# Kernel optimization log

Measured on AMD Instinct MI355X. Metric: run time of the kernel, lower is better.

The kernel has to match this reference:

```python
import jax, jax.numpy as jnp
import numpy as np


def lstm_step(x_t, h, c, Wih, Whh, bih, bhh):
    # PyTorch LSTM gate order: i, f, g, o
    gates = x_t @ Wih.T + h @ Whh.T + bih + bhh
    i, f, g, o = jnp.split(gates, 4, axis=-1)
    i = jax.nn.sigmoid(i)
    f = jax.nn.sigmoid(f)
    g = jnp.tanh(g)
    o = jax.nn.sigmoid(o)
    c_new = f * c + i * g
    h_new = o * jnp.tanh(c_new)
    return h_new, c_new


def setup_inputs() -> dict:
    key = jax.random.key(0)
    N, C, T, V, M = 512, 3, 300, 25, 2
    F = C * V * M  # 150
    H = 100
    ks = jax.random.split(key, 12)
    s = 1.0 / np.sqrt(H)  # PyTorch LSTM/Linear init scale
    u = lambda k, shape: jax.random.uniform(k, shape, jnp.float32, -s, s)
    return {
        "x": jax.random.normal(ks[0], (N, C, T, V, M), jnp.float32),
        "enc_Wih": u(ks[1], (4 * H, F)),
        "enc_Whh": u(ks[2], (4 * H, H)),
        "enc_bih": u(ks[3], (4 * H,)),
        "enc_bhh": u(ks[4], (4 * H,)),
        "dec_Wih": u(ks[5], (4 * H, F)),
        "dec_Whh": u(ks[6], (4 * H, H)),
        "dec_bih": u(ks[7], (4 * H,)),
        "dec_bhh": u(ks[8], (4 * H,)),
        "fc_W": u(ks[9], (F, H)),
        "fc_b": u(ks[10], (F,)),
    }


def reference(x, enc_Wih, enc_Whh, enc_bih, enc_bhh,
              dec_Wih, dec_Whh, dec_bih, dec_bhh, fc_W, fc_b):
    N, C, T, V, M = x.shape
    F = C * V * M
    H = enc_Whh.shape[1]
    # (N,C,T,V,M) -> (N,T,C*V*M)
    xs = jnp.transpose(x, (0, 2, 1, 3, 4)).reshape(N, T, F)

    # Encoder LSTM: only need final (h, c)
    h0 = jnp.zeros((N, H), x.dtype)
    c0 = jnp.zeros((N, H), x.dtype)

    def enc_step(carry, xt):
        h, c = carry
        h, c = lstm_step(xt, h, c, enc_Wih, enc_Whh, enc_bih, enc_bhh)
        return (h, c), None

    (h, c), _ = jax.lax.scan(enc_step, (h0, c0), jnp.swapaxes(xs, 0, 1))

    inp0 = jnp.zeros((N, F), x.dtype)

    def dec_step(carry, _):
        inp, h, c = carry
        h, c = lstm_step(inp, h, c, dec_Wih, dec_Whh, dec_bih, dec_bhh)
        out = h @ fc_W.T + fc_b
        return (out, h, c), out

    _, outs = jax.lax.scan(dec_step, (inp0, h, c), None, length=T - 1)  # [T-1,N,F]

    # outputs[:,0,:] stays zero, like the torch.zeros buffer
    outputs = jnp.concatenate([jnp.zeros((1, N, F), x.dtype), outs], axis=0)  # [T,N,F]
    outputs = jnp.swapaxes(outputs, 0, 1).reshape(N, T, C, V, M)
    return jnp.transpose(outputs, (0, 2, 1, 3, 4))  # (N,C,T,V,M)
```

## Files before the change

### kernel.cpp

```cpp
#include <hip/hip_runtime.h>
#include <hip/hip_fp16.h>


#define B_W2P   0u
#define B_WDP   102400u
#define B_WEP   204800u
#define B_PIH   307200u
#define B_BENC  460800u
#define B_B1    462848u
#define B_BEFF  464896u
#define B_HIST  466944u
#define HIST_STRIDE 29952
#define B_XG    31137792u

typedef _Float16 h2_t __attribute__((ext_vector_type(2)));

#if defined(__has_builtin)
#if __has_builtin(__builtin_amdgcn_fdot2)
#define HAS_FDOT2 1
#endif
#endif

__device__ __forceinline__ float fdot2u(unsigned a, unsigned b, float c) {
#ifdef HAS_FDOT2
  return __builtin_amdgcn_fdot2(__builtin_bit_cast(h2_t, a), __builtin_bit_cast(h2_t, b), c, false);
#else
  float al = __half2float(__ushort_as_half((unsigned short)(a & 0xffffu)));
  float ah = __half2float(__ushort_as_half((unsigned short)(a >> 16)));
  float bl = __half2float(__ushort_as_half((unsigned short)(b & 0xffffu)));
  float bh = __half2float(__ushort_as_half((unsigned short)(b >> 16)));
  return fmaf(ah, bh, fmaf(al, bl, c));
#endif
}

__device__ __forceinline__ unsigned pack2f(float a, float b) {
  return (unsigned)__half_as_ushort(__float2half(a)) |
         ((unsigned)__half_as_ushort(__float2half(b)) << 16);
}

__device__ __forceinline__ float fast_sig(float x) {
  float e = __builtin_amdgcn_exp2f(x * -1.442695040888963f);
  return __builtin_amdgcn_rcpf(1.f + e);
}
__device__ __forceinline__ float fast_tanh(float x) {
  float e = __builtin_amdgcn_exp2f(x * -2.885390081777926f);
  return fmaf(2.f, __builtin_amdgcn_rcpf(1.f + e), -1.f);
}

__device__ __forceinline__ float lstm_tail(float acc, int ty, float& c) {
  float sg = fast_sig(acc);
  float th = fast_tanh(acc);
  float act = (ty == 2) ? th : sg;
  float v1 = __shfl_xor(act, 1);
  float v2 = __shfl_xor(act, 2);
  float v3 = __shfl_xor(v1, 2);
  c = fmaf(v1, c, act * v2);
  return v3 * fast_tanh(c);
}

__device__ __forceinline__ float dot100(const unsigned short* hb, const unsigned* wp) {
  const uint4* h4 = (const uint4*)hb;
  float a0 = 0.f, a1 = 0.f, a2 = 0.f, a3 = 0.f;
#pragma unroll
  for (int ch = 0; ch < 12; ++ch) {
    uint4 v = h4[ch];
    a0 = fdot2u(wp[4 * ch + 0], v.x, a0);
    a1 = fdot2u(wp[4 * ch + 1], v.y, a1);
    a2 = fdot2u(wp[4 * ch + 2], v.z, a2);
    a3 = fdot2u(wp[4 * ch + 3], v.w, a3);
  }
  uint2 v2 = *(const uint2*)(hb + 96);
  a0 = fdot2u(wp[48], v2.x, a0);
  a1 = fdot2u(wp[49], v2.y, a1);
  return (a0 + a1) + (a2 + a3);
}

__global__ void prep(const float* __restrict__ dWih, const float* __restrict__ dWhh,
                     const float* __restrict__ dbih, const float* __restrict__ dbhh,
                     const float* __restrict__ eWih, const float* __restrict__ eWhh,
                     const float* __restrict__ ebih, const float* __restrict__ ebhh,
                     const float* __restrict__ fcW,  const float* __restrict__ fcb,
                     char* __restrict__ wsb)
{
  int idx = blockIdx.x * 256 + threadIdx.x;
  if (idx < 25600) {
    int q = idx >> 9, t = idx & 511;
    unsigned w2p = 0, wdp = 0, wep = 0;
    if (t < 400) {
      int r = (t & 3) * 100 + (t >> 2);
      int j0 = 2 * q, j1 = 2 * q + 1;
      float wd0 = dWhh[r * 100 + j0], wd1 = dWhh[r * 100 + j1];
      float we0 = eWhh[r * 100 + j0], we1 = eWhh[r * 100 + j1];
      float s0 = 0.f, s1 = 0.f;
      for (int f = 0; f < 150; ++f) {
        float a = dWih[r * 150 + f];
        s0 = fmaf(a, fcW[f * 100 + j0], s0);
        s1 = fmaf(a, fcW[f * 100 + j1], s1);
      }
      w2p = pack2f(wd0 + s0, wd1 + s1);
      wdp = pack2f(wd0, wd1);
      wep = pack2f(we0, we1);
    }
    ((unsigned*)(wsb + B_W2P))[idx] = w2p;
    ((unsigned*)(wsb + B_WDP))[idx] = wdp;
    ((unsigned*)(wsb + B_WEP))[idx] = wep;
  } else if (idx < 25600 + 38400) {
    int k = idx - 25600; int d = k >> 9, t = k & 511;
    unsigned pk = 0;
    if (t < 400) {
      int r = (t & 3) * 100 + (t >> 2);
      pk = pack2f(eWih[r * 150 + 2 * d], eWih[r * 150 + 2 * d + 1]);
    }
    ((unsigned*)(wsb + B_PIH))[k] = pk;
  } else if (idx < 25600 + 38400 + 512) {
    int t = idx - (25600 + 38400);
    float be = 0.f, b1 = 0.f, bf = 0.f;
    if (t < 400) {
      int r = (t & 3) * 100 + (t >> 2);
      be = ebih[r] + ebhh[r];
      b1 = dbih[r] + dbhh[r];
      float acc = 0.f;
      for (int f = 0; f < 150; ++f) acc = fmaf(dWih[r * 150 + f], fcb[f], acc);
      bf = b1 + acc;
    }
    ((float*)(wsb + B_BENC))[t] = be;
    ((float*)(wsb + B_B1))[t]   = b1;
    ((float*)(wsb + B_BEFF))[t] = bf;
  }
}

__global__ __launch_bounds__(512, 4)
void pre(const float* __restrict__ x, const char* __restrict__ wsb,
         unsigned short* __restrict__ xg, int n0)
{
  const int tid = threadIdx.x;
  const int n = n0 + blockIdx.x;
  __shared__ unsigned short xls[150 * 160];

  unsigned wih[75];
  const unsigned* pih = (const unsigned*)(wsb + B_PIH);
#pragma unroll
  for (int d = 0; d < 75; ++d) wih[d] = pih[(d << 9) + tid];

  const float* xb = x + (size_t)n * 45000;
  unsigned short* xgr = xg + (size_t)blockIdx.x * 120000 + ((tid < 400) ? tid : 0);
  const bool on = tid < 400;

  for (int phase = 0; phase < 2; ++phase) {
    const int tbase = phase * 150;
    if (phase) __syncthreads();
    for (int d = tid; d < 150 * 160; d += 512) {
      int tl = d / 160, f = d - tl * 160;
      float v = 0.f;
      if (f < 150) {
        int c = f / 50, q = f - c * 50;
        v = xb[c * 15000 + (tbase + tl) * 50 + q];
      }
      xls[tl * 160 + f] = __half_as_ushort(__float2half(v));
    }
    __syncthreads();
    if (on) {
      for (int tl = 0; tl < 150; ++tl) {
        const uint4* row = (const uint4*)(xls + tl * 160);
        float a0 = 0.f, a1 = 0.f, a2 = 0.f, a3 = 0.f;
#pragma unroll
        for (int ch = 0; ch < 18; ++ch) {
          uint4 v = row[ch];
          a0 = fdot2u(wih[4 * ch + 0], v.x, a0);
          a1 = fdot2u(wih[4 * ch + 1], v.y, a1);
          a2 = fdot2u(wih[4 * ch + 2], v.z, a2);
          a3 = fdot2u(wih[4 * ch + 3], v.w, a3);
        }
        uint4 v = row[18];
        a0 = fdot2u(wih[72], v.x, a0);
        a1 = fdot2u(wih[73], v.y, a1);
        a2 = fdot2u(wih[74], v.z, a2);
        float a = (a0 + a1) + (a2 + a3);
        xgr[(size_t)(tbase + tl) * 400] = __half_as_ushort(__float2half(a));
      }
    }
  }
}

__global__ __launch_bounds__(512, 4)
void recurrent(const unsigned short* __restrict__ xg, char* __restrict__ wsb, int n0)
{
  const int t  = threadIdx.x;
  const int n  = n0 + blockIdx.x;
  const int j  = t >> 2, ty = t & 3;
  const bool leader = (t < 400) && (ty == 0);
  __shared__ unsigned short hh[2][112];

  const unsigned* WEP = (const unsigned*)(wsb + B_WEP);
  const unsigned* WDP = (const unsigned*)(wsb + B_WDP);
  const unsigned* W2P = (const unsigned*)(wsb + B_W2P);

  unsigned wp[50];
#pragma unroll
  for (int q = 0; q < 50; ++q) wp[q] = WEP[(q << 9) + t];

  const float benc = ((const float*)(wsb + B_BENC))[t];
  const float b1g  = ((const float*)(wsb + B_B1))[t];
  const float beff = ((const float*)(wsb + B_BEFF))[t];
  unsigned short* histn = (unsigned short*)(wsb + B_HIST) + (size_t)n * HIST_STRIDE;
  const unsigned short* xgr = xg + (size_t)blockIdx.x * 120000 + ((t < 400) ? t : 0);
  float c = 0.f;

  unsigned short p1 = xgr[400];
  {
    float acc = benc + __half2float(__ushort_as_half(xgr[0]));
    float hn = lstm_tail(acc, ty, c);
    if (leader) hh[1][j] = __half_as_ushort(__float2half(hn));
    __syncthreads();
  }
  for (int ts = 1; ts < 300; ++ts) {
    const int rd = ts & 1, wr = rd ^ 1;
    unsigned short pn = xgr[(size_t)((ts + 1 < 300) ? ts + 1 : 299) * 400];
    float acc = benc + __half2float(__ushort_as_half(p1)) + dot100(hh[rd], wp);
    float hn = lstm_tail(acc, ty, c);
    if (leader) hh[wr][j] = __half_as_ushort(__float2half(hn));
    __syncthreads();
    p1 = pn;
  }

#pragma unroll
  for (int q = 0; q < 50; ++q) wp[q] = WDP[(q << 9) + t];
  {
    float acc = b1g + dot100(hh[0], wp);
    float hn = lstm_tail(acc, ty, c);
    if (leader) {
      hh[1][j] = __half_as_ushort(__float2half(hn));
      histn[j] = __half_as_ushort(__float2half(hn));
    }
    __syncthreads();
  }
#pragma unroll
  for (int q = 0; q < 50; ++q) wp[q] = W2P[(q << 9) + t];
  for (int s = 2; s <= 299; ++s) {
    const int rd = (299 + s) & 1, wr = rd ^ 1;
    float acc = beff + dot100(hh[rd], wp);
    float hn = lstm_tail(acc, ty, c);
    if (leader) {
      hh[wr][j] = __half_as_ushort(__float2half(hn));
      histn[(s - 1) * 100 + j] = __half_as_ushort(__float2half(hn));
    }
    __syncthreads();
  }
}

__global__ __launch_bounds__(192, 4)
void emit(const char* __restrict__ wsb, const float* __restrict__ fcW,
          const float* __restrict__ fcb, float* __restrict__ out)
{
  const int f = threadIdx.x;
  const int n = blockIdx.x;
  const int z = blockIdx.y;
  __shared__ unsigned short hl[15008];

  const uint4* src = (const uint4*)((const unsigned short*)(wsb + B_HIST) +
                                    (size_t)n * HIST_STRIDE + z * 15000);
  for (int k = f; k < 1875; k += 192) ((uint4*)hl)[k] = src[k];

  const bool on = f < 150;
  unsigned fw[50];
  float bias = 0.f;
  if (on) {
    const float* fp = fcW + f * 100;
#pragma unroll
    for (int q = 0; q < 50; ++q) fw[q] = pack2f(fp[2 * q], fp[2 * q + 1]);
    bias = fcb[f];
  }
  __syncthreads();

  if (!on) return;
  const int cc = f / 50, r = f - cc * 50;
  float* ob = out + (size_t)n * 45000 + cc * 15000 + r;
  if (z == 0) ob[0] = 0.f;
  const int rows = z ? 149 : 150;
  for (int tl = 0; tl < rows; ++tl) {
    const uint4* row = (const uint4*)(hl + tl * 100);
    float a0 = bias, a1 = 0.f, a2 = 0.f, a3 = 0.f;
#pragma unroll
    for (int ch = 0; ch < 12; ++ch) {
      uint4 v = row[ch];
      a0 = fdot2u(fw[4 * ch + 0], v.x, a0);
      a1 = fdot2u(fw[4 * ch + 1], v.y, a1);
      a2 = fdot2u(fw[4 * ch + 2], v.z, a2);
      a3 = fdot2u(fw[4 * ch + 3], v.w, a3);
    }
    uint2 v2 = *(const uint2*)(hl + tl * 100 + 96);
    a0 = fdot2u(fw[48], v2.x, a0);
    a1 = fdot2u(fw[49], v2.y, a1);
    const int tt = z * 150 + tl + 1;
    ob[tt * 50] = (a0 + a1) + (a2 + a3);
  }
}

extern "C" void kernel_launch(void* const* d_in, const int* in_sizes, int n_in,
                              void* d_out, int out_size, void* d_ws, size_t ws_size,
                              hipStream_t stream) {
  const float* x    = (const float*)d_in[0];
  const float* eWih = (const float*)d_in[1];
  const float* eWhh = (const float*)d_in[2];
  const float* ebih = (const float*)d_in[3];
  const float* ebhh = (const float*)d_in[4];
  const float* dWih = (const float*)d_in[5];
  const float* dWhh = (const float*)d_in[6];
  const float* dbih = (const float*)d_in[7];
  const float* dbhh = (const float*)d_in[8];
  const float* fcW  = (const float*)d_in[9];
  const float* fcb  = (const float*)d_in[10];
  float* out = (float*)d_out;
  char* wsb  = (char*)d_ws;

  int npass = 1;
  while (npass < 8) {
    size_t need = (size_t)B_XG + (size_t)(512 / npass) * 300 * 400 * 2;
    if (need <= ws_size) break;
    npass *= 2;
  }
  const int chunk = 512 / npass;
  unsigned short* xg = (unsigned short*)(wsb + B_XG);

  prep<<<252, 256, 0, stream>>>(dWih, dWhh, dbih, dbhh, eWih, eWhh, ebih, ebhh, fcW, fcb, wsb);
  for (int p = 0; p < npass; ++p) {
    pre<<<chunk, 512, 0, stream>>>(x, wsb, xg, p * chunk);
    recurrent<<<chunk, 512, 0, stream>>>(xg, wsb, p * chunk);
  }
  emit<<<dim3(512, 2), 192, 0, stream>>>(wsb, fcW, fcb, out);
}
```

Baseline: 1.141 ms.

## Split encoder along time into two halves over all sequences instead of batch passes

Instead of running the pre/recurrent pair once per batch chunk, sized to the workspace, the encoder input projection and recurrence are split into two time halves of 150 steps. Each half launches all 512 sequences at once, and the h and c state is saved to and restored from the history area between the halves. This keeps the xg buffer at half the full size while giving every launch the whole batch, which cuts the serial recurrent step chain when multiple passes were needed before. It costs an extra launch pair plus a state save and reload when the workspace could previously hold the whole buffer in one pass. It also no longer checks ws_size.

Result: slower. 1.219 ms (+6.8%).

```diff
diff --git a/kernel.cpp b/kernel.cpp
--- a/kernel.cpp
+++ b/kernel.cpp
@@ -131,10 +131,10 @@
 
 __global__ __launch_bounds__(512, 4)
 void pre(const float* __restrict__ x, const char* __restrict__ wsb,
-         unsigned short* __restrict__ xg, int n0)
+         unsigned short* __restrict__ xg, int tbase)
 {
   const int tid = threadIdx.x;
-  const int n = n0 + blockIdx.x;
+  const int n = blockIdx.x;
   __shared__ unsigned short xls[150 * 160];
 
   unsigned wih[75];
@@ -143,50 +143,46 @@
   for (int d = 0; d < 75; ++d) wih[d] = pih[(d << 9) + tid];
 
   const float* xb = x + (size_t)n * 45000;
-  unsigned short* xgr = xg + (size_t)blockIdx.x * 120000 + ((tid < 400) ? tid : 0);
+  unsigned short* xgr = xg + (size_t)n * 60000 + ((tid < 400) ? tid : 0);
   const bool on = tid < 400;
 
-  for (int phase = 0; phase < 2; ++phase) {
-    const int tbase = phase * 150;
-    if (phase) __syncthreads();
-    for (int d = tid; d < 150 * 160; d += 512) {
-      int tl = d / 160, f = d - tl * 160;
-      float v = 0.f;
-      if (f < 150) {
-        int c = f / 50, q = f - c * 50;
-        v = xb[c * 15000 + (tbase + tl) * 50 + q];
+  for (int d = tid; d < 150 * 160; d += 512) {
+    int tl = d / 160, f = d - tl * 160;
+    float v = 0.f;
+    if (f < 150) {
+      int c = f / 50, q = f - c * 50;
+      v = xb[c * 15000 + (tbase + tl) * 50 + q];
+    }
+    xls[tl * 160 + f] = __half_as_ushort(__float2half(v));
+  }
+  __syncthreads();
+  if (on) {
+    for (int tl = 0; tl < 150; ++tl) {
+      const uint4* row = (const uint4*)(xls + tl * 160);
+      float a0 = 0.f, a1 = 0.f, a2 = 0.f, a3 = 0.f;
+#pragma unroll
+      for (int ch = 0; ch < 18; ++ch) {
+        uint4 v = row[ch];
+        a0 = fdot2u(wih[4 * ch + 0], v.x, a0);
+        a1 = fdot2u(wih[4 * ch + 1], v.y, a1);
+        a2 = fdot2u(wih[4 * ch + 2], v.z, a2);
+        a3 = fdot2u(wih[4 * ch + 3], v.w, a3);
       }
-      xls[tl * 160 + f] = __half_as_ushort(__float2half(v));
-    }
-    __syncthreads();
-    if (on) {
-      for (int tl = 0; tl < 150; ++tl) {
-        const uint4* row = (const uint4*)(xls + tl * 160);
-        float a0 = 0.f, a1 = 0.f, a2 = 0.f, a3 = 0.f;
-#pragma unroll
-        for (int ch = 0; ch < 18; ++ch) {
-          uint4 v = row[ch];
-          a0 = fdot2u(wih[4 * ch + 0], v.x, a0);
-          a1 = fdot2u(wih[4 * ch + 1], v.y, a1);
-          a2 = fdot2u(wih[4 * ch + 2], v.z, a2);
-          a3 = fdot2u(wih[4 * ch + 3], v.w, a3);
-        }
-        uint4 v = row[18];
-        a0 = fdot2u(wih[72], v.x, a0);
-        a1 = fdot2u(wih[73], v.y, a1);
-        a2 = fdot2u(wih[74], v.z, a2);
-        float a = (a0 + a1) + (a2 + a3);
-        xgr[(size_t)(tbase + tl) * 400] = __half_as_ushort(__float2half(a));
-      }
+      uint4 v = row[18];
+      a0 = fdot2u(wih[72], v.x, a0);
+      a1 = fdot2u(wih[73], v.y, a1);
+      a2 = fdot2u(wih[74], v.z, a2);
+      float a = (a0 + a1) + (a2 + a3);
+      xgr[(size_t)tl * 400] = __half_as_ushort(__float2half(a));
     }
   }
 }
 
 __global__ __launch_bounds__(512, 4)
-void recurrent(const unsigned short* __restrict__ xg, char* __restrict__ wsb, int n0)
+void recurrent(const unsigned short* __restrict__ xg, char* __restrict__ wsb, int phase)
 {
   const int t  = threadIdx.x;
-  const int n  = n0 + blockIdx.x;
+  const int n  = blockIdx.x;
   const int j  = t >> 2, ty = t & 3;
   const bool leader = (t < 400) && (ty == 0);
   __shared__ unsigned short hh[2][112];
@@ -203,19 +199,41 @@
   const float b1g  = ((const float*)(wsb + B_B1))[t];
   const float beff = ((const float*)(wsb + B_BEFF))[t];
   unsigned short* histn = (unsigned short*)(wsb + B_HIST) + (size_t)n * HIST_STRIDE;
-  const unsigned short* xgr = xg + (size_t)blockIdx.x * 120000 + ((t < 400) ? t : 0);
+  float* stc = (float*)(histn + 128);
+  const unsigned short* xgr = xg + (size_t)n * 60000 + ((t < 400) ? t : 0);
   float c = 0.f;
 
-  unsigned short p1 = xgr[400];
-  {
-    float acc = benc + __half2float(__ushort_as_half(xgr[0]));
-    float hn = lstm_tail(acc, ty, c);
-    if (leader) hh[1][j] = __half_as_ushort(__float2half(hn));
-    __syncthreads();
-  }
-  for (int ts = 1; ts < 300; ++ts) {
+  if (phase == 0) {
+    unsigned short p1 = xgr[400];
+    {
+      float acc = benc + __half2float(__ushort_as_half(xgr[0]));
+      float hn = lstm_tail(acc, ty, c);
+      if (leader) hh[1][j] = __half_as_ushort(__float2half(hn));
+      __syncthreads();
+    }
+    for (int ts = 1; ts < 150; ++ts) {
+      const int rd = ts & 1, wr = rd ^ 1;
+      unsigned short pn = xgr[(size_t)((ts + 1 < 150) ? ts + 1 : 149) * 400];
+      float acc = benc + __half2float(__ushort_as_half(p1)) + dot100(hh[rd], wp);
+      float hn = lstm_tail(acc, ty, c);
+      if (leader) hh[wr][j] = __half_as_ushort(__float2half(hn));
+      __syncthreads();
+      p1 = pn;
+    }
+    if (t < 100) histn[t] = hh[0][t];
+    if (leader)  stc[j] = c;
+    return;
+  }
+
+  if (t < 100) hh[0][t] = histn[t];
+  if (t < 400) c = stc[j];
+  unsigned short p1 = xgr[0];
+  __syncthreads();
+
+  for (int ts = 150; ts < 300; ++ts) {
     const int rd = ts & 1, wr = rd ^ 1;
-    unsigned short pn = xgr[(size_t)((ts + 1 < 300) ? ts + 1 : 299) * 400];
+    const int idx = ts - 150;
+    unsigned short pn = xgr[(size_t)((idx + 1 < 150) ? idx + 1 : 149) * 400];
     float acc = benc + __half2float(__ushort_as_half(p1)) + dot100(hh[rd], wp);
     float hn = lstm_tail(acc, ty, c);
     if (leader) hh[wr][j] = __half_as_ushort(__float2half(hn));
@@ -313,19 +331,12 @@
   float* out = (float*)d_out;
   char* wsb  = (char*)d_ws;
 
-  int npass = 1;
-  while (npass < 8) {
-    size_t need = (size_t)B_XG + (size_t)(512 / npass) * 300 * 400 * 2;
-    if (need <= ws_size) break;
-    npass *= 2;
-  }
-  const int chunk = 512 / npass;
   unsigned short* xg = (unsigned short*)(wsb + B_XG);
 
   prep<<<252, 256, 0, stream>>>(dWih, dWhh, dbih, dbhh, eWih, eWhh, ebih, ebhh, fcW, fcb, wsb);
-  for (int p = 0; p < npass; ++p) {
-    pre<<<chunk, 512, 0, stream>>>(x, wsb, xg, p * chunk);
-    recurrent<<<chunk, 512, 0, stream>>>(xg, wsb, p * chunk);
-  }
+  pre<<<512, 512, 0, stream>>>(x, wsb, xg, 0);
+  recurrent<<<512, 512, 0, stream>>>(xg, wsb, 0);
+  pre<<<512, 512, 0, stream>>>(x, wsb, xg, 150);
+  recurrent<<<512, 512, 0, stream>>>(xg, wsb, 1);
   emit<<<dim3(512, 2), 192, 0, stream>>>(wsb, fcW, fcb, out);
 }
```

## Batch 16 samples per block with MFMA and fuse input projection into recurrence

Applied to the files above, without the earlier changes.

The separate input-projection kernel and its fp16 gate buffer in workspace are removed. The recurrent kernel now processes 16 batch samples per block. It concatenates h and x_t along K and computes all gates with 16x16x32 f16 MFMA instructions, while raw x for the next step is prefetched and converted into shared memory. This removes the large intermediate write and read and the extra launch, and moves the gate matvec onto the matrix cores. The cost is a grid of only 32 blocks, which uses few CUs, plus wider per-step work on each wave.

Result: slower. 1.200 ms (+5.1%).

```diff
diff --git a/kernel.cpp b/kernel.cpp
--- a/kernel.cpp
+++ b/kernel.cpp
@@ -11,9 +11,10 @@
 #define B_BEFF  464896u
 #define B_HIST  466944u
 #define HIST_STRIDE 29952
-#define B_XG    31137792u
 
 typedef _Float16 h2_t __attribute__((ext_vector_type(2)));
+typedef _Float16 f16x8 __attribute__((ext_vector_type(8)));
+typedef float f32x4v __attribute__((ext_vector_type(4)));
 
 #if defined(__has_builtin)
 #if __has_builtin(__builtin_amdgcn_fdot2)
@@ -47,32 +48,9 @@
   return fmaf(2.f, __builtin_amdgcn_rcpf(1.f + e), -1.f);
 }
 
-__device__ __forceinline__ float lstm_tail(float acc, int ty, float& c) {
-  float sg = fast_sig(acc);
-  float th = fast_tanh(acc);
-  float act = (ty == 2) ? th : sg;
-  float v1 = __shfl_xor(act, 1);
-  float v2 = __shfl_xor(act, 2);
-  float v3 = __shfl_xor(v1, 2);
-  c = fmaf(v1, c, act * v2);
-  return v3 * fast_tanh(c);
-}
-
-__device__ __forceinline__ float dot100(const unsigned short* hb, const unsigned* wp) {
-  const uint4* h4 = (const uint4*)hb;
-  float a0 = 0.f, a1 = 0.f, a2 = 0.f, a3 = 0.f;
-#pragma unroll
-  for (int ch = 0; ch < 12; ++ch) {
-    uint4 v = h4[ch];
-    a0 = fdot2u(wp[4 * ch + 0], v.x, a0);
-    a1 = fdot2u(wp[4 * ch + 1], v.y, a1);
-    a2 = fdot2u(wp[4 * ch + 2], v.z, a2);
-    a3 = fdot2u(wp[4 * ch + 3], v.w, a3);
-  }
-  uint2 v2 = *(const uint2*)(hb + 96);
-  a0 = fdot2u(wp[48], v2.x, a0);
-  a1 = fdot2u(wp[49], v2.y, a1);
-  return (a0 + a1) + (a2 + a3);
+__device__ __forceinline__ f32x4v mfma16(uint4 a, uint4 b, f32x4v c) {
+  return __builtin_amdgcn_mfma_f32_16x16x32_f16(
+      __builtin_bit_cast(f16x8, a), __builtin_bit_cast(f16x8, b), c, 0, 0, 0);
 }
 
 __global__ void prep(const float* __restrict__ dWih, const float* __restrict__ dWhh,
@@ -129,120 +107,192 @@
   }
 }
 
-__global__ __launch_bounds__(512, 4)
-void pre(const float* __restrict__ x, const char* __restrict__ wsb,
-         unsigned short* __restrict__ xg, int n0)
+__global__ __launch_bounds__(448, 2)
+void recurrent(const float* __restrict__ x, char* __restrict__ wsb)
 {
-  const int tid = threadIdx.x;
-  const int n = n0 + blockIdx.x;
-  __shared__ unsigned short xls[150 * 160];
-
-  unsigned wih[75];
-  const unsigned* pih = (const unsigned*)(wsb + B_PIH);
-#pragma unroll
-  for (int d = 0; d < 75; ++d) wih[d] = pih[(d << 9) + tid];
-
-  const float* xb = x + (size_t)n * 45000;
-  unsigned short* xgr = xg + (size_t)blockIdx.x * 120000 + ((tid < 400) ? tid : 0);
-  const bool on = tid < 400;
-
-  for (int phase = 0; phase < 2; ++phase) {
-    const int tbase = phase * 150;
-    if (phase) __syncthreads();
-    for (int d = tid; d < 150 * 160; d += 512) {
-      int tl = d / 160, f = d - tl * 160;
-      float v = 0.f;
-      if (f < 150) {
-        int c = f / 50, q = f - c * 50;
-        v = xb[c * 15000 + (tbase + tl) * 50 + q];
-      }
-      xls[tl * 160 + f] = __half_as_ushort(__float2half(v));
-    }
-    __syncthreads();
-    if (on) {
-      for (int tl = 0; tl < 150; ++tl) {
-        const uint4* row = (const uint4*)(xls + tl * 160);
-        float a0 = 0.f, a1 = 0.f, a2 = 0.f, a3 = 0.f;
-#pragma unroll
-        for (int ch = 0; ch < 18; ++ch) {
-          uint4 v = row[ch];
-          a0 = fdot2u(wih[4 * ch + 0], v.x, a0);
-          a1 = fdot2u(wih[4 * ch + 1], v.y, a1);
-          a2 = fdot2u(wih[4 * ch + 2], v.z, a2);
-          a3 = fdot2u(wih[4 * ch + 3], v.w, a3);
-        }
-        uint4 v = row[18];
-        a0 = fdot2u(wih[72], v.x, a0);
-        a1 = fdot2u(wih[73], v.y, a1);
-        a2 = fdot2u(wih[74], v.z, a2);
-        float a = (a0 + a1) + (a2 + a3);
-        xgr[(size_t)(tbase + tl) * 400] = __half_as_ushort(__float2half(a));
-      }
-    }
-  }
-}
-
-__global__ __launch_bounds__(512, 4)
-void recurrent(const unsigned short* __restrict__ xg, char* __restrict__ wsb, int n0)
-{
-  const int t  = threadIdx.x;
-  const int n  = n0 + blockIdx.x;
-  const int j  = t >> 2, ty = t & 3;
-  const bool leader = (t < 400) && (ty == 0);
-  __shared__ unsigned short hh[2][112];
+  const int tid  = threadIdx.x;
+  const int w    = tid >> 6;
+  const int lane = tid & 63;
+  const int sp   = lane & 15;
+  const int q    = lane >> 4;
+  const int nb   = blockIdx.x * 16;
+
+  __shared__ unsigned short hx[2][16][264];
+  for (int k = tid; k < 2 * 16 * 264; k += 448) ((unsigned short*)hx)[k] = 0;
 
   const unsigned* WEP = (const unsigned*)(wsb + B_WEP);
   const unsigned* WDP = (const unsigned*)(wsb + B_WDP);
   const unsigned* W2P = (const unsigned*)(wsb + B_W2P);
-
-  unsigned wp[50];
-#pragma unroll
-  for (int q = 0; q < 50; ++q) wp[q] = WEP[(q << 9) + t];
-
-  const float benc = ((const float*)(wsb + B_BENC))[t];
-  const float b1g  = ((const float*)(wsb + B_B1))[t];
-  const float beff = ((const float*)(wsb + B_BEFF))[t];
-  unsigned short* histn = (unsigned short*)(wsb + B_HIST) + (size_t)n * HIST_STRIDE;
-  const unsigned short* xgr = xg + (size_t)blockIdx.x * 120000 + ((t < 400) ? t : 0);
-  float c = 0.f;
-
-  unsigned short p1 = xgr[400];
+  const unsigned* PIH = (const unsigned*)(wsb + B_PIH);
+
+  const int nt = (w < 4) ? 4 : 3;
+  int cells[4];
+  float4 bs[4];
+  uint4 af[4][8];
+#pragma unroll
+  for (int i = 0; i < 4; ++i) {
+    const int tile = (i < nt) ? (w + 7 * i) : 0;
+    const int col = tile * 16 + sp;
+    cells[i] = 4 * tile + q;
+#pragma unroll
+    for (int kk = 0; kk < 8; ++kk) {
+      unsigned e[4];
+#pragma unroll
+      for (int l = 0; l < 4; ++l) {
+        const int p = kk * 16 + q * 4 + l;
+        unsigned v = 0u;
+        if (p < 50) v = WEP[p * 512 + col];
+        else if (p < 125) v = PIH[(p - 50) * 512 + col];
+        e[l] = v;
+      }
+      af[i][kk] = make_uint4(e[0], e[1], e[2], e[3]);
+    }
+    bs[i] = ((const float4*)(wsb + B_BENC))[cells[i]];
+  }
+
+  const bool stg = tid < 400;
+  const int ssp = tid / 25;
+  const int sr  = tid - ssp * 25;
+  const float* xb = x + (size_t)(nb + (stg ? ssp : 0)) * 45000;
+  int soff[6];
+#pragma unroll
+  for (int l = 0; l < 6; ++l) {
+    const int f = sr * 6 + l;
+    const int cd = f / 50;
+    soff[l] = cd * 15000 + (f - cd * 50);
+  }
+  const int sdst = (stg ? ssp : 0) * 264 + 100 + sr * 6;
+
+  unsigned short* histn = (unsigned short*)(wsb + B_HIST) + (size_t)(nb + sp) * HIST_STRIDE;
+
+  __syncthreads();
+  if (stg) {
+    float xv[6];
+#pragma unroll
+    for (int l = 0; l < 6; ++l) xv[l] = xb[soff[l]];
+    unsigned short* d = &hx[0][0][0] + sdst;
+    *(unsigned*)(d + 0) = pack2f(xv[0], xv[1]);
+    *(unsigned*)(d + 2) = pack2f(xv[2], xv[3]);
+    *(unsigned*)(d + 4) = pack2f(xv[4], xv[5]);
+  }
+  __syncthreads();
+
+  float cst[4] = {0.f, 0.f, 0.f, 0.f};
+
+  for (int t = 0; t < 300; ++t) {
+    const int rd = t & 1, wr = rd ^ 1;
+    const bool pf = stg && (t < 299);
+    float xv[6];
+    if (pf) {
+      const int to = (t + 1) * 50;
+#pragma unroll
+      for (int l = 0; l < 6; ++l) xv[l] = xb[soff[l] + to];
+    }
+    f32x4v acc[4];
+#pragma unroll
+    for (int i = 0; i < 4; ++i) {
+      acc[i][0] = bs[i].x; acc[i][1] = bs[i].y;
+      acc[i][2] = bs[i].z; acc[i][3] = bs[i].w;
+    }
+#pragma unroll
+    for (int kk = 0; kk < 8; ++kk) {
+      uint4 b = *(const uint4*)(&hx[rd][sp][kk * 32 + q * 8]);
+#pragma unroll
+      for (int i = 0; i < 4; ++i)
+        if (i < nt) acc[i] = mfma16(af[i][kk], b, acc[i]);
+    }
+#pragma unroll
+    for (int i = 0; i < 4; ++i) {
+      if (i < nt) {
+        float ii = fast_sig(acc[i][0]), ff = fast_sig(acc[i][1]);
+        float gg = fast_tanh(acc[i][2]), oo = fast_sig(acc[i][3]);
+        cst[i] = fmaf(ff, cst[i], ii * gg);
+        float h = oo * fast_tanh(cst[i]);
+        hx[wr][sp][cells[i]] = __half_as_ushort(__float2half(h));
+      }
+    }
+    if (pf) {
+      unsigned short* d = &hx[wr][0][0] + sdst;
+      *(unsigned*)(d + 0) = pack2f(xv[0], xv[1]);
+      *(unsigned*)(d + 2) = pack2f(xv[2], xv[3]);
+      *(unsigned*)(d + 4) = pack2f(xv[4], xv[5]);
+    }
+    __syncthreads();
+  }
+
+  auto loadA4 = [&](const unsigned* W, unsigned bofs) {
+#pragma unroll
+    for (int i = 0; i < 4; ++i) {
+      const int tile = (i < nt) ? (w + 7 * i) : 0;
+      const int col = tile * 16 + sp;
+#pragma unroll
+      for (int kk = 0; kk < 4; ++kk) {
+        unsigned e[4];
+#pragma unroll
+        for (int l = 0; l < 4; ++l) {
+          const int p = kk * 16 + q * 4 + l;
+          e[l] = (p < 50) ? W[p * 512 + col] : 0u;
+        }
+        af[i][kk] = make_uint4(e[0], e[1], e[2], e[3]);
+      }
+      bs[i] = ((const float4*)(wsb + bofs))[cells[i]];
+    }
+  };
+
+  loadA4(WDP, B_B1);
   {
-    float acc = benc + __half2float(__ushort_as_half(xgr[0]));
-    float hn = lstm_tail(acc, ty, c);
-    if (leader) hh[1][j] = __half_as_ushort(__float2half(hn));
+    f32x4v acc[4];
+#pragma unroll
+    for (int i = 0; i < 4; ++i) {
+      acc[i][0] = bs[i].x; acc[i][1] = bs[i].y;
+      acc[i][2] = bs[i].z; acc[i][3] = bs[i].w;
+    }
+#pragma unroll
+    for (int kk = 0; kk < 4; ++kk) {
+      uint4 b = *(const uint4*)(&hx[0][sp][kk * 32 + q * 8]);
+#pragma unroll
+      for (int i = 0; i < 4; ++i)
+        if (i < nt) acc[i] = mfma16(af[i][kk], b, acc[i]);
+    }
+#pragma unroll
+    for (int i = 0; i < 4; ++i) {
+      if (i < nt) {
+        float ii = fast_sig(acc[i][0]), ff = fast_sig(acc[i][1]);
+        float gg = fast_tanh(acc[i][2]), oo = fast_sig(acc[i][3]);
+        cst[i] = fmaf(ff, cst[i], ii * gg);
+        float h = oo * fast_tanh(cst[i]);
+        hx[1][sp][cells[i]] = __half_as_ushort(__float2half(h));
+        histn[cells[i]] = __half_as_ushort(__float2half(h));
+      }
+    }
     __syncthreads();
   }
-  for (int ts = 1; ts < 300; ++ts) {
-    const int rd = ts & 1, wr = rd ^ 1;
-    unsigned short pn = xgr[(size_t)((ts + 1 < 300) ? ts + 1 : 299) * 400];
-    float acc = benc + __half2float(__ushort_as_half(p1)) + dot100(hh[rd], wp);
-    float hn = lstm_tail(acc, ty, c);
-    if (leader) hh[wr][j] = __half_as_ushort(__float2half(hn));
-    __syncthreads();
-    p1 = pn;
-  }
-
-#pragma unroll
-  for (int q = 0; q < 50; ++q) wp[q] = WDP[(q << 9) + t];
-  {
-    float acc = b1g + dot100(hh[0], wp);
-    float hn = lstm_tail(acc, ty, c);
-    if (leader) {
-      hh[1][j] = __half_as_ushort(__float2half(hn));
-      histn[j] = __half_as_ushort(__float2half(hn));
-    }
-    __syncthreads();
-  }
-#pragma unroll
-  for (int q = 0; q < 50; ++q) wp[q] = W2P[(q << 9) + t];
+  loadA4(W2P, B_BEFF);
   for (int s = 2; s <= 299; ++s) {
     const int rd = (299 + s) & 1, wr = rd ^ 1;
-    float acc = beff + dot100(hh[rd], wp);
-    float hn = lstm_tail(acc, ty, c);
-    if (leader) {
-      hh[wr][j] = __half_as_ushort(__float2half(hn));
-      histn[(s - 1) * 100 + j] = __half_as_ushort(__float2half(hn));
+    f32x4v acc[4];
+#pragma unroll
+    for (int i = 0; i < 4; ++i) {
+      acc[i][0] = bs[i].x; acc[i][1] = bs[i].y;
+      acc[i][2] = bs[i].z; acc[i][3] = bs[i].w;
+    }
+#pragma unroll
+    for (int kk = 0; kk < 4; ++kk) {
+      uint4 b = *(const uint4*)(&hx[rd][sp][kk * 32 + q * 8]);
+#pragma unroll
+      for (int i = 0; i < 4; ++i)
+        if (i < nt) acc[i] = mfma16(af[i][kk], b, acc[i]);
+    }
+#pragma unroll
+    for (int i = 0; i < 4; ++i) {
+      if (i < nt) {
+        float ii = fast_sig(acc[i][0]), ff = fast_sig(acc[i][1]);
+        float gg = fast_tanh(acc[i][2]), oo = fast_sig(acc[i][3]);
+        cst[i] = fmaf(ff, cst[i], ii * gg);
+        float h = oo * fast_tanh(cst[i]);
+        hx[wr][sp][cells[i]] = __half_as_ushort(__float2half(h));
+        histn[(s - 1) * 100 + cells[i]] = __half_as_ushort(__float2half(h));
+      }
     }
     __syncthreads();
   }
@@ -313,19 +363,7 @@
   float* out = (float*)d_out;
   char* wsb  = (char*)d_ws;
 
-  int npass = 1;
-  while (npass < 8) {
-    size_t need = (size_t)B_XG + (size_t)(512 / npass) * 300 * 400 * 2;
-    if (need <= ws_size) break;
-    npass *= 2;
-  }
-  const int chunk = 512 / npass;
-  unsigned short* xg = (unsigned short*)(wsb + B_XG);
-
   prep<<<252, 256, 0, stream>>>(dWih, dWhh, dbih, dbhh, eWih, eWhh, ebih, ebhh, fcW, fcb, wsb);
-  for (int p = 0; p < npass; ++p) {
-    pre<<<chunk, 512, 0, stream>>>(x, wsb, xg, p * chunk);
-    recurrent<<<chunk, 512, 0, stream>>>(xg, wsb, p * chunk);
-  }
+  recurrent<<<32, 448, 0, stream>>>(x, wsb);
   emit<<<dim3(512, 2), 192, 0, stream>>>(wsb, fcW, fcb, out);
 }
```
